# Optimization experiments

Measured on AMD Instinct MI355X. Metric: run time of the kernel, lower is better.

Reference implementation:

```python
import jax, jax.numpy as jnp
import numpy as np

DIM = 2048
N_HEADS = 32
N_KV_HEADS = 8
HEAD_DIM = DIM // N_HEADS  # 64
SEQ = 2048
BATCH = 2


def _rope_freqs(seq_len, head_dim, theta=10000.0):
    inv = 1.0 / (theta ** (np.arange(0, head_dim, 2)[: head_dim // 2].astype(np.float32) / head_dim))
    t = np.arange(seq_len, dtype=np.float32)
    ang = np.outer(t, inv)  # (seq, head_dim//2)
    return jnp.asarray(np.cos(ang)), jnp.asarray(np.sin(ang))


def setup_inputs() -> dict:
    key = jax.random.key(0)
    ks = jax.random.split(key, 5)
    x = jax.random.normal(ks[0], (BATCH, SEQ, DIM), dtype=jnp.float32)
    s = 1.0 / np.sqrt(DIM)
    wq = jax.random.normal(ks[1], (N_HEADS * HEAD_DIM, DIM), dtype=jnp.float32) * s
    wk = jax.random.normal(ks[2], (N_KV_HEADS * HEAD_DIM, DIM), dtype=jnp.float32) * s
    wv = jax.random.normal(ks[3], (N_KV_HEADS * HEAD_DIM, DIM), dtype=jnp.float32) * s
    wo = jax.random.normal(ks[4], (DIM, N_HEADS * HEAD_DIM), dtype=jnp.float32) * s
    freqs_cos, freqs_sin = _rope_freqs(SEQ, HEAD_DIM)
    return {"x": x, "freqs_cos": freqs_cos, "freqs_sin": freqs_sin,
            "wq": wq, "wk": wk, "wv": wv, "wo": wo}


def _apply_rope(t, cos, sin):
    # t: (B, S, H, D); cos/sin: (S, D//2) broadcast to (1, S, 1, D//2)
    B, S, H, D = t.shape
    tr = t.reshape(B, S, H, D // 2, 2)
    x0, x1 = tr[..., 0], tr[..., 1]
    c = cos[None, :, None, :]
    s = sin[None, :, None, :]
    o0 = x0 * c - x1 * s
    o1 = x0 * s + x1 * c
    return jnp.stack([o0, o1], axis=-1).reshape(B, S, H, D)


def reference(x, freqs_cos, freqs_sin, wq, wk, wv, wo):
    B, S, _ = x.shape
    H, KV, D = N_HEADS, N_KV_HEADS, HEAD_DIM
    rep = H // KV
    xq = jnp.einsum('bsd,hd->bsh', x, wq).reshape(B, S, H, D)
    xk = jnp.einsum('bsd,hd->bsh', x, wk).reshape(B, S, KV, D)
    xv = jnp.einsum('bsd,hd->bsh', x, wv).reshape(B, S, KV, D)
    xq = _apply_rope(xq, freqs_cos, freqs_sin)
    xk = _apply_rope(xk, freqs_cos, freqs_sin)
    # GQA without materializing repeated K/V: group q heads as (KV, rep).
    # repeat_interleave on dim=2 maps q head h -> kv head h // rep.
    xqg = xq.reshape(B, S, KV, rep, D)
    scale = 1.0 / jnp.sqrt(jnp.float32(D))
    scores = jnp.einsum('bqkrd,bskd->bkrqs', xqg, xk) * scale  # (B,KV,rep,S,S)
    causal = jnp.tril(jnp.ones((S, S), dtype=bool))
    scores = jnp.where(causal[None, None, None], scores, jnp.float32(-jnp.inf))
    probs = jax.nn.softmax(scores, axis=-1)
    out = jnp.einsum('bkrqs,bskd->bqkrd', probs, xv)  # (B,S,KV,rep,D)
    out = out.reshape(B, S, H * D)
    return jnp.einsum('bsh,dh->bsd', out, wo)
```

## Files before the change

### kernel.cpp

```cpp
#include <hip/hip_runtime.h>

#define DIMSZ 2048
#define NH 32
#define NKV 8
#define HD 64
#define SEQLEN 2048
#define BATCH 2
#define NROWS (BATCH*SEQLEN)
#define NQKVC 3072

typedef __bf16 bf16x8 __attribute__((ext_vector_type(8)));
typedef float f32x4v __attribute__((ext_vector_type(4)));

__device__ __forceinline__ unsigned short f2bf(float f) {
  union { float f; unsigned int u; } v; v.f = f;
  return (unsigned short)((v.u + 0x7FFFu + ((v.u >> 16) & 1u)) >> 16);
}
__device__ __forceinline__ float bf2f(unsigned int bits16) {
  union { unsigned int u; float f; } v; v.u = bits16 << 16; return v.f;
}
__device__ __forceinline__ int swz128(int row, int colBytes) {
  return row * 128 + (colBytes ^ ((row & 7) << 4));
}

#define GLOAD16(g, l) __builtin_amdgcn_global_load_lds( \
    (const __attribute__((address_space(1))) unsigned int*)(g), \
    (__attribute__((address_space(3))) unsigned int*)(l), 16, 0, 0)

__global__ void k_cvt(const float* __restrict__ s, unsigned short* __restrict__ d, int n4) {
  int i = blockIdx.x * 256 + threadIdx.x;
  if (i >= n4) return;
  float4 v = reinterpret_cast<const float4*>(s)[i];
  unsigned long long pk =
      (unsigned long long)f2bf(v.x) |
      ((unsigned long long)f2bf(v.y) << 16) |
      ((unsigned long long)f2bf(v.z) << 32) |
      ((unsigned long long)f2bf(v.w) << 48);
  reinterpret_cast<unsigned long long*>(d)[i] = pk;
}

__global__ void k_cvt_w(const float* __restrict__ wq, const float* __restrict__ wk,
                        const float* __restrict__ wv, unsigned short* __restrict__ d) {
  int i = blockIdx.x * 256 + threadIdx.x;
  const float* s; int off;
  if (i < 1048576)      { s = wq; off = i; }
  else if (i < 1310720) { s = wk; off = i - 1048576; }
  else                  { s = wv; off = i - 1310720; }
  float4 v = reinterpret_cast<const float4*>(s)[off];
  unsigned long long pk =
      (unsigned long long)f2bf(v.x) |
      ((unsigned long long)f2bf(v.y) << 16) |
      ((unsigned long long)f2bf(v.z) << 32) |
      ((unsigned long long)f2bf(v.w) << 48);
  reinterpret_cast<unsigned long long*>(d)[i] = pk;
}

template<int OUT_BF16>
__global__ __launch_bounds__(256, 2) void k_gemm_bt(
    const unsigned short* __restrict__ A,
    const unsigned short* __restrict__ B,
    void* __restrict__ Cv, int M, int N, int K)
{
  constexpr int BK = 64;
  __shared__ __attribute__((aligned(16))) unsigned short smA[128 * BK];
  __shared__ __attribute__((aligned(16))) unsigned short smB[128 * BK];
  const int tid = threadIdx.x;
  const int lane = tid & 63;
  const int wid = tid >> 6;
  const int lr = lane & 15, lg = lane >> 4;
  const int gx = gridDim.x;
  int lin = blockIdx.y * gx + blockIdx.x;
  const int cpx = (gx * gridDim.y) >> 3;
  lin = (lin & 7) * cpx + (lin >> 3);
  const int m0 = (lin / gx) * 128, n0 = (lin % gx) * 128;
  const int wr = (wid >> 1) * 64, wc = (wid & 1) * 64;

  f32x4v acc[4][4];
  #pragma unroll
  for (int i = 0; i < 4; i++)
    #pragma unroll
    for (int j = 0; j < 4; j++)
      acc[i][j] = f32x4v{0.f, 0.f, 0.f, 0.f};

  for (int k0 = 0; k0 < K; k0 += BK) {
    #pragma unroll
    for (int c = 0; c < 4; c++) {
      const int chunk = wid * 4 + c;
      const int idx = chunk * 64 + lane;
      const int row = idx >> 3, s = idx & 7;
      const int ks = (s ^ (row & 7)) * 8;
      GLOAD16(A + (size_t)(m0 + row) * K + k0 + ks, &smA[chunk * 512]);
      GLOAD16(B + (size_t)(n0 + row) * K + k0 + ks, &smB[chunk * 512]);
    }
    __syncthreads();
    #pragma unroll
    for (int ks = 0; ks < 2; ks++) {
      bf16x8 af[4], bfv[4];
      #pragma unroll
      for (int m = 0; m < 4; m++)
        af[m] = *reinterpret_cast<const bf16x8*>((char*)smA + swz128(wr + m * 16 + lr, ks * 64 + lg * 16));
      #pragma unroll
      for (int n = 0; n < 4; n++)
        bfv[n] = *reinterpret_cast<const bf16x8*>((char*)smB + swz128(wc + n * 16 + lr, ks * 64 + lg * 16));
      #pragma unroll
      for (int m = 0; m < 4; m++)
        #pragma unroll
        for (int n = 0; n < 4; n++)
          acc[m][n] = __builtin_amdgcn_mfma_f32_16x16x32_bf16(af[m], bfv[n], acc[m][n], 0, 0, 0);
    }
    __syncthreads();
  }
  #pragma unroll
  for (int m = 0; m < 4; m++)
    #pragma unroll
    for (int n = 0; n < 4; n++)
      #pragma unroll
      for (int r = 0; r < 4; r++) {
        const size_t row = m0 + wr + m * 16 + lg * 4 + r;
        const size_t col = n0 + wc + n * 16 + lr;
        if (OUT_BF16) ((unsigned short*)Cv)[row * N + col] = f2bf(acc[m][n][r]);
        else          ((float*)Cv)[row * N + col] = acc[m][n][r];
      }
}

__global__ void k_rope_q(const unsigned short* __restrict__ qkv,
                         const float* __restrict__ fc, const float* __restrict__ fs,
                         unsigned short* __restrict__ Qb)
{
  const int tid = blockIdx.x * 256 + threadIdx.x;
  const int i = tid & 31;
  const int t2 = tid >> 5;
  const int h = t2 & 31;
  const int row = t2 >> 5;
  const int s = row & (SEQLEN - 1);
  const int b = row >> 11;
  const unsigned int u = *reinterpret_cast<const unsigned int*>(qkv + (size_t)row * NQKVC + h * HD + 2 * i);
  const float x0 = bf2f(u & 0xffffu), x1 = bf2f(u >> 16);
  const float c = fc[s * 32 + i], sn = fs[s * 32 + i];
  const float SCL = 0.18033688011112043f;
  const float o0 = (x0 * c - x1 * sn) * SCL;
  const float o1 = (x0 * sn + x1 * c) * SCL;
  const unsigned int pk = (unsigned int)f2bf(o0) | ((unsigned int)f2bf(o1) << 16);
  *reinterpret_cast<unsigned int*>(Qb + ((size_t)((b * NH + h) * SEQLEN + s)) * HD + 2 * i) = pk;
}

__global__ void k_rope_k(const unsigned short* __restrict__ qkv,
                         const float* __restrict__ fc, const float* __restrict__ fs,
                         unsigned short* __restrict__ Kb)
{
  const int tid = blockIdx.x * 256 + threadIdx.x;
  const int i = tid & 31;
  const int t2 = tid >> 5;
  const int kv = t2 & 7;
  const int row = t2 >> 3;
  const int s = row & (SEQLEN - 1);
  const int b = row >> 11;
  const unsigned int u = *reinterpret_cast<const unsigned int*>(
      qkv + (size_t)row * NQKVC + DIMSZ + kv * HD + 2 * i);
  const float x0 = bf2f(u & 0xffffu), x1 = bf2f(u >> 16);
  const float c = fc[s * 32 + i], sn = fs[s * 32 + i];
  const float o0 = x0 * c - x1 * sn;
  const float o1 = x0 * sn + x1 * c;
  const unsigned int pk = (unsigned int)f2bf(o0) | ((unsigned int)f2bf(o1) << 16);
  *reinterpret_cast<unsigned int*>(Kb + ((size_t)((b * NKV + kv) * SEQLEN + s)) * HD + 2 * i) = pk;
}

__global__ void k_vt(const unsigned short* __restrict__ qkv, unsigned short* __restrict__ Vt) {
  __shared__ unsigned short tile[64][72];
  const int st = blockIdx.x, kv = blockIdx.y, b = blockIdx.z;
  const int tid = threadIdx.x;
  #pragma unroll
  for (int j2 = 0; j2 < 2; j2++) {
    const int s = (tid >> 3) + j2 * 32, dc = (tid & 7) * 8;
    const int row = b * SEQLEN + st * 64 + s;
    uint4 v = *reinterpret_cast<const uint4*>(
        qkv + (size_t)row * NQKVC + DIMSZ + NKV * HD + kv * HD + dc);
    const unsigned short* vs = reinterpret_cast<const unsigned short*>(&v);
    #pragma unroll
    for (int j = 0; j < 8; j++) tile[s][dc + j] = vs[j];
  }
  __syncthreads();
  {
    const int d = tid >> 2, sc = (tid & 3) * 16;
    unsigned short tmp[16];
    #pragma unroll
    for (int j = 0; j < 16; j++) tmp[j] = tile[sc + j][d];
    unsigned short* outp = Vt + ((size_t)((b * NKV + kv) * HD) + d) * SEQLEN + st * 64 + sc;
    *reinterpret_cast<uint4*>(outp)     = *reinterpret_cast<uint4*>(tmp);
    *reinterpret_cast<uint4*>(outp + 8) = *reinterpret_cast<uint4*>(tmp + 8);
  }
}

__global__ __launch_bounds__(512, 2) void k_attn(
    const unsigned short* __restrict__ Qg,
    const unsigned short* __restrict__ Kg,
    const unsigned short* __restrict__ Vt,
    unsigned short* __restrict__ Og)
{
  constexpr int KVB = 64;
  __shared__ __attribute__((aligned(16))) unsigned short sK[KVB * HD];
  __shared__ __attribute__((aligned(16))) unsigned short sV[HD * KVB];
  __shared__ __attribute__((aligned(16))) unsigned short sP[8 * 16 * KVB];
  const int tid = threadIdx.x;
  const int lane = tid & 63, wid = tid >> 6;
  const int lr = lane & 15, lg = lane >> 4;
  const int orig = blockIdx.x;
  const int w = (orig & 7) * 64 + (orig >> 3);
  const int kvh = w >> 6;
  const int b = (w >> 5) & 1;
  const int h = kvh * 4 + ((w >> 3) & 3);
  const int qp = w & 7;
  const unsigned short* Qp = Qg + ((size_t)(b * NH + h) * SEQLEN) * HD;
  const unsigned short* Kp = Kg + ((size_t)(b * NKV + kvh) * SEQLEN) * HD;
  const unsigned short* Vp = Vt + ((size_t)(b * NKV + kvh) * HD) * SEQLEN;
  unsigned short* Pw = sP + wid * (16 * KVB);

  const int sidx = wid * 64 + lane;
  const int srow = sidx >> 3;
  const int scol = ((sidx & 7) ^ (srow & 7)) * 8;

  for (int phase = 0; phase < 2; phase++) {
    const int qt = phase ? (15 - qp) : qp;
    const int qrow0 = qt * 128 + wid * 16;
    bf16x8 aq[2];
    #pragma unroll
    for (int ks = 0; ks < 2; ks++)
      aq[ks] = *reinterpret_cast<const bf16x8*>(Qp + (size_t)(qrow0 + lr) * HD + ks * 32 + lg * 8);

    f32x4v accO[4];
    #pragma unroll
    for (int r = 0; r < 4; r++) accO[r] = f32x4v{0.f, 0.f, 0.f, 0.f};
    float mrun = -3.0e38f, lrun = 0.f;

    const int nt = qt * 2 + 2;
    for (int t = 0; t < nt; t++) {
      const int kv0 = t * KVB;
      GLOAD16(Kp + (size_t)(kv0 + srow) * HD + scol, &sK[wid * 512]);
      GLOAD16(Vp + (size_t)srow * SEQLEN + kv0 + scol, &sV[wid * 512]);
      __syncthreads();
      if (kv0 <= qrow0 + 15) {
        f32x4v sfr[4];
        #pragma unroll
        for (int c = 0; c < 4; c++) sfr[c] = f32x4v{0.f, 0.f, 0.f, 0.f};
        __builtin_amdgcn_s_setprio(1);
        #pragma unroll
        for (int ks = 0; ks < 2; ks++) {
          bf16x8 bk[4];
          #pragma unroll
          for (int c = 0; c < 4; c++)
            bk[c] = *reinterpret_cast<const bf16x8*>((char*)sK + swz128(c * 16 + lr, ks * 64 + lg * 16));
          #pragma unroll
          for (int c = 0; c < 4; c++)
            sfr[c] = __builtin_amdgcn_mfma_f32_16x16x32_bf16(bk[c], aq[ks], sfr[c], 0, 0, 0);
        }
        __builtin_amdgcn_s_setprio(0);
        if (kv0 + KVB - 1 > qrow0) {
          const int q = qrow0 + lr;
          #pragma unroll
          for (int c = 0; c < 4; c++)
            #pragma unroll
            for (int r = 0; r < 4; r++) {
              const int kv = kv0 + c * 16 + lg * 4 + r;
              if (kv > q) sfr[c][r] = -1.0e30f;
            }
        }
        float mc[4];
        #pragma unroll
        for (int c = 0; c < 4; c++)
          mc[c] = fmaxf(fmaxf(sfr[c][0], sfr[c][1]), fmaxf(sfr[c][2], sfr[c][3]));
        float tm = fmaxf(fmaxf(mc[0], mc[1]), fmaxf(mc[2], mc[3]));
        tm = fmaxf(tm, __shfl_xor(tm, 16));
        tm = fmaxf(tm, __shfl_xor(tm, 32));
        const float mo = mrun;
        const bool defer = __all(tm <= mo + 8.0f);
        const float mn = defer ? mo : fmaxf(mo, tm);
        float rc[4];
        #pragma unroll
        for (int c = 0; c < 4; c++) {
          float p0 = __builtin_amdgcn_exp2f(sfr[c][0] - mn);
          float p1 = __builtin_amdgcn_exp2f(sfr[c][1] - mn);
          float p2 = __builtin_amdgcn_exp2f(sfr[c][2] - mn);
          float p3 = __builtin_amdgcn_exp2f(sfr[c][3] - mn);
          sfr[c][0] = p0; sfr[c][1] = p1; sfr[c][2] = p2; sfr[c][3] = p3;
          rc[c] = (p0 + p1) + (p2 + p3);
        }
        float rs = (rc[0] + rc[1]) + (rc[2] + rc[3]);
        rs += __shfl_xor(rs, 16);
        rs += __shfl_xor(rs, 32);
        if (defer) {
          lrun += rs;
        } else {
          const float sc = __builtin_amdgcn_exp2f(mo - mn);
          mrun = mn;
          lrun = lrun * sc + rs;
          #pragma unroll
          for (int r = 0; r < 4; r++) {
            const float scr = __shfl(sc, (lg << 4) + (lg << 2) + r);
            #pragma unroll
            for (int dc = 0; dc < 4; dc++) accO[dc][r] *= scr;
          }
        }
        #pragma unroll
        for (int c = 0; c < 4; c++) {
          uint2 pk;
          pk.x = (unsigned int)f2bf(sfr[c][0]) | ((unsigned int)f2bf(sfr[c][1]) << 16);
          pk.y = (unsigned int)f2bf(sfr[c][2]) | ((unsigned int)f2bf(sfr[c][3]) << 16);
          *reinterpret_cast<uint2*>((char*)Pw + swz128(lr, c * 32 + lg * 8)) = pk;
        }
        __builtin_amdgcn_s_setprio(1);
        #pragma unroll
        for (int ks = 0; ks < 2; ks++) {
          bf16x8 ap = *reinterpret_cast<const bf16x8*>((char*)Pw + swz128(lr, ks * 64 + lg * 16));
          bf16x8 bv[4];
          #pragma unroll
          for (int dc = 0; dc < 4; dc++)
            bv[dc] = *reinterpret_cast<const bf16x8*>((char*)sV + swz128(dc * 16 + lr, ks * 64 + lg * 16));
          #pragma unroll
          for (int dc = 0; dc < 4; dc++)
            accO[dc] = __builtin_amdgcn_mfma_f32_16x16x32_bf16(ap, bv[dc], accO[dc], 0, 0, 0);
        }
        __builtin_amdgcn_s_setprio(0);
      }
      __syncthreads();
    }
    const float inv = 1.0f / lrun;
    #pragma unroll
    for (int r = 0; r < 4; r++) {
      const float invr = __shfl(inv, (lg << 4) + (lg << 2) + r);
      const int q = qrow0 + lg * 4 + r;
      #pragma unroll
      for (int dc = 0; dc < 4; dc++) {
        const int d = dc * 16 + lr;
        Og[(size_t)(b * SEQLEN + q) * DIMSZ + h * HD + d] = f2bf(accO[dc][r] * invr);
      }
    }
  }
}

extern "C" void kernel_launch(void* const* d_in, const int* in_sizes, int n_in,
                              void* d_out, int out_size, void* d_ws, size_t ws_size,
                              hipStream_t stream)
{
  const float* x  = (const float*)d_in[0];
  const float* fc = (const float*)d_in[1];
  const float* fs = (const float*)d_in[2];
  const float* wq = (const float*)d_in[3];
  const float* wk = (const float*)d_in[4];
  const float* wv = (const float*)d_in[5];
  const float* wo = (const float*)d_in[6];
  float* out = (float*)d_out;
  char* ws = (char*)d_ws;

  unsigned short* xb    = (unsigned short*)(ws + 0);
  unsigned short* wqkvb = (unsigned short*)(ws + 16777216);
  unsigned short* wob   = (unsigned short*)(ws + 29360128);
  unsigned short* qkv   = (unsigned short*)(ws + 37748736);
  unsigned short* Qb    = (unsigned short*)(ws + 62914560);
  unsigned short* Kb    = (unsigned short*)(ws + 79691776);
  unsigned short* Vtb   = (unsigned short*)(ws + 83886080);
  unsigned short* attnb = (unsigned short*)(ws + 88080384);

  k_cvt<<<8192, 256, 0, stream>>>(x,  xb, 2097152);
  k_cvt_w<<<6144, 256, 0, stream>>>(wq, wk, wv, wqkvb);
  k_cvt<<<4096, 256, 0, stream>>>(wo, wob, 1048576);

  dim3 g1(24, 32);
  k_gemm_bt<1><<<g1, 256, 0, stream>>>(xb, wqkvb, qkv, NROWS, NQKVC, DIMSZ);

  k_rope_q<<<16384, 256, 0, stream>>>(qkv, fc, fs, Qb);
  k_rope_k<<<4096, 256, 0, stream>>>(qkv, fc, fs, Kb);
  dim3 gv(32, 8, 2);
  k_vt<<<gv, 256, 0, stream>>>(qkv, Vtb);

  k_attn<<<512, 512, 0, stream>>>(Qb, Kb, Vtb, attnb);

  dim3 g2(16, 32);
  k_gemm_bt<0><<<g2, 256, 0, stream>>>(attnb, wob, out, NROWS, DIMSZ, DIMSZ);
}
```

Measured before the change: 196.7 us.

## Double-buffer K/V tiles in attention and use hardware bf16 pack conversion

The attention kernel now keeps two LDS buffers for K and V and issues the async global-to-LDS load for the next KV tile before computing on the current one. This overlaps memory latency with MFMA and softmax work and removes one barrier per tile. It also replaces the manual round-to-nearest bf16 bit trick with compiler bf16 conversions, including a packed two-element convert, in all conversion paths. The cost is double the K/V LDS footprint, which may affect occupancy at 2 blocks per CU, and the change relies on the load-then-barrier ordering being correct.

```diff
diff --git a/kernel.cpp b/kernel.cpp
--- a/kernel.cpp
+++ b/kernel.cpp
@@ -10,11 +10,18 @@
 #define NQKVC 3072
 
 typedef __bf16 bf16x8 __attribute__((ext_vector_type(8)));
+typedef __bf16 bf16x2 __attribute__((ext_vector_type(2)));
 typedef float f32x4v __attribute__((ext_vector_type(4)));
+typedef float f32x2v __attribute__((ext_vector_type(2)));
 
 __device__ __forceinline__ unsigned short f2bf(float f) {
-  union { float f; unsigned int u; } v; v.f = f;
-  return (unsigned short)((v.u + 0x7FFFu + ((v.u >> 16) & 1u)) >> 16);
+  __bf16 h = (__bf16)f;
+  union { __bf16 h; unsigned short u; } v; v.h = h; return v.u;
+}
+__device__ __forceinline__ unsigned int pk2bf(float lo, float hi) {
+  f32x2v v; v[0] = lo; v[1] = hi;
+  bf16x2 h = __builtin_convertvector(v, bf16x2);
+  union { bf16x2 h; unsigned int u; } c; c.h = h; return c.u;
 }
 __device__ __forceinline__ float bf2f(unsigned int bits16) {
   union { unsigned int u; float f; } v; v.u = bits16 << 16; return v.f;
@@ -31,12 +38,8 @@
   int i = blockIdx.x * 256 + threadIdx.x;
   if (i >= n4) return;
   float4 v = reinterpret_cast<const float4*>(s)[i];
-  unsigned long long pk =
-      (unsigned long long)f2bf(v.x) |
-      ((unsigned long long)f2bf(v.y) << 16) |
-      ((unsigned long long)f2bf(v.z) << 32) |
-      ((unsigned long long)f2bf(v.w) << 48);
-  reinterpret_cast<unsigned long long*>(d)[i] = pk;
+  uint2 pk; pk.x = pk2bf(v.x, v.y); pk.y = pk2bf(v.z, v.w);
+  reinterpret_cast<uint2*>(d)[i] = pk;
 }
 
 __global__ void k_cvt_w(const float* __restrict__ wq, const float* __restrict__ wk,
@@ -47,12 +50,8 @@
   else if (i < 1310720) { s = wk; off = i - 1048576; }
   else                  { s = wv; off = i - 1310720; }
   float4 v = reinterpret_cast<const float4*>(s)[off];
-  unsigned long long pk =
-      (unsigned long long)f2bf(v.x) |
-      ((unsigned long long)f2bf(v.y) << 16) |
-      ((unsigned long long)f2bf(v.z) << 32) |
-      ((unsigned long long)f2bf(v.w) << 48);
-  reinterpret_cast<unsigned long long*>(d)[i] = pk;
+  uint2 pk; pk.x = pk2bf(v.x, v.y); pk.y = pk2bf(v.z, v.w);
+  reinterpret_cast<uint2*>(d)[i] = pk;
 }
 
 template<int OUT_BF16>
@@ -140,8 +139,7 @@
   const float SCL = 0.18033688011112043f;
   const float o0 = (x0 * c - x1 * sn) * SCL;
   const float o1 = (x0 * sn + x1 * c) * SCL;
-  const unsigned int pk = (unsigned int)f2bf(o0) | ((unsigned int)f2bf(o1) << 16);
-  *reinterpret_cast<unsigned int*>(Qb + ((size_t)((b * NH + h) * SEQLEN + s)) * HD + 2 * i) = pk;
+  *reinterpret_cast<unsigned int*>(Qb + ((size_t)((b * NH + h) * SEQLEN + s)) * HD + 2 * i) = pk2bf(o0, o1);
 }
 
 __global__ void k_rope_k(const unsigned short* __restrict__ qkv,
@@ -161,8 +159,7 @@
   const float c = fc[s * 32 + i], sn = fs[s * 32 + i];
   const float o0 = x0 * c - x1 * sn;
   const float o1 = x0 * sn + x1 * c;
-  const unsigned int pk = (unsigned int)f2bf(o0) | ((unsigned int)f2bf(o1) << 16);
-  *reinterpret_cast<unsigned int*>(Kb + ((size_t)((b * NKV + kv) * SEQLEN + s)) * HD + 2 * i) = pk;
+  *reinterpret_cast<unsigned int*>(Kb + ((size_t)((b * NKV + kv) * SEQLEN + s)) * HD + 2 * i) = pk2bf(o0, o1);
 }
 
 __global__ void k_vt(const unsigned short* __restrict__ qkv, unsigned short* __restrict__ Vt) {
@@ -198,8 +195,10 @@
     unsigned short* __restrict__ Og)
 {
   constexpr int KVB = 64;
-  __shared__ __attribute__((aligned(16))) unsigned short sK[KVB * HD];
-  __shared__ __attribute__((aligned(16))) unsigned short sV[HD * KVB];
+  __shared__ __attribute__((aligned(16))) unsigned short sK0[KVB * HD];
+  __shared__ __attribute__((aligned(16))) unsigned short sK1[KVB * HD];
+  __shared__ __attribute__((aligned(16))) unsigned short sV0[HD * KVB];
+  __shared__ __attribute__((aligned(16))) unsigned short sV1[HD * KVB];
   __shared__ __attribute__((aligned(16))) unsigned short sP[8 * 16 * KVB];
   const int tid = threadIdx.x;
   const int lane = tid & 63, wid = tid >> 6;
@@ -232,95 +231,109 @@
     for (int r = 0; r < 4; r++) accO[r] = f32x4v{0.f, 0.f, 0.f, 0.f};
     float mrun = -3.0e38f, lrun = 0.f;
 
-    const int nt = qt * 2 + 2;
-    for (int t = 0; t < nt; t++) {
-      const int kv0 = t * KVB;
-      GLOAD16(Kp + (size_t)(kv0 + srow) * HD + scol, &sK[wid * 512]);
-      GLOAD16(Vp + (size_t)srow * SEQLEN + kv0 + scol, &sV[wid * 512]);
-      __syncthreads();
-      if (kv0 <= qrow0 + 15) {
-        f32x4v sfr[4];
-        #pragma unroll
-        for (int c = 0; c < 4; c++) sfr[c] = f32x4v{0.f, 0.f, 0.f, 0.f};
-        __builtin_amdgcn_s_setprio(1);
-        #pragma unroll
-        for (int ks = 0; ks < 2; ks++) {
-          bf16x8 bk[4];
-          #pragma unroll
-          for (int c = 0; c < 4; c++)
-            bk[c] = *reinterpret_cast<const bf16x8*>((char*)sK + swz128(c * 16 + lr, ks * 64 + lg * 16));
-          #pragma unroll
-          for (int c = 0; c < 4; c++)
-            sfr[c] = __builtin_amdgcn_mfma_f32_16x16x32_bf16(bk[c], aq[ks], sfr[c], 0, 0, 0);
-        }
-        __builtin_amdgcn_s_setprio(0);
-        if (kv0 + KVB - 1 > qrow0) {
-          const int q = qrow0 + lr;
-          #pragma unroll
-          for (int c = 0; c < 4; c++)
-            #pragma unroll
-            for (int r = 0; r < 4; r++) {
-              const int kv = kv0 + c * 16 + lg * 4 + r;
-              if (kv > q) sfr[c][r] = -1.0e30f;
-            }
-        }
-        float mc[4];
+    auto compute = [&](int kv0, auto& sKb, auto& sVb) {
+      if (kv0 > qrow0 + 15) return;
+      f32x4v sfr[4];
+      #pragma unroll
+      for (int c = 0; c < 4; c++) sfr[c] = f32x4v{0.f, 0.f, 0.f, 0.f};
+      __builtin_amdgcn_s_setprio(1);
+      #pragma unroll
+      for (int ks = 0; ks < 2; ks++) {
+        bf16x8 bk[4];
         #pragma unroll
         for (int c = 0; c < 4; c++)
-          mc[c] = fmaxf(fmaxf(sfr[c][0], sfr[c][1]), fmaxf(sfr[c][2], sfr[c][3]));
-        float tm = fmaxf(fmaxf(mc[0], mc[1]), fmaxf(mc[2], mc[3]));
-        tm = fmaxf(tm, __shfl_xor(tm, 16));
-        tm = fmaxf(tm, __shfl_xor(tm, 32));
-        const float mo = mrun;
-        const bool defer = __all(tm <= mo + 8.0f);
-        const float mn = defer ? mo : fmaxf(mo, tm);
-        float rc[4];
-        #pragma unroll
-        for (int c = 0; c < 4; c++) {
-          float p0 = __builtin_amdgcn_exp2f(sfr[c][0] - mn);
-          float p1 = __builtin_amdgcn_exp2f(sfr[c][1] - mn);
-          float p2 = __builtin_amdgcn_exp2f(sfr[c][2] - mn);
-          float p3 = __builtin_amdgcn_exp2f(sfr[c][3] - mn);
-          sfr[c][0] = p0; sfr[c][1] = p1; sfr[c][2] = p2; sfr[c][3] = p3;
-          rc[c] = (p0 + p1) + (p2 + p3);
-        }
-        float rs = (rc[0] + rc[1]) + (rc[2] + rc[3]);
-        rs += __shfl_xor(rs, 16);
-        rs += __shfl_xor(rs, 32);
-        if (defer) {
-          lrun += rs;
-        } else {
-          const float sc = __builtin_amdgcn_exp2f(mo - mn);
-          mrun = mn;
-          lrun = lrun * sc + rs;
+          bk[c] = *reinterpret_cast<const bf16x8*>((char*)sKb + swz128(c * 16 + lr, ks * 64 + lg * 16));
+        #pragma unroll
+        for (int c = 0; c < 4; c++)
+          sfr[c] = __builtin_amdgcn_mfma_f32_16x16x32_bf16(bk[c], aq[ks], sfr[c], 0, 0, 0);
+      }
+      __builtin_amdgcn_s_setprio(0);
+      if (kv0 + KVB - 1 > qrow0) {
+        const int q = qrow0 + lr;
+        #pragma unroll
+        for (int c = 0; c < 4; c++)
           #pragma unroll
           for (int r = 0; r < 4; r++) {
-            const float scr = __shfl(sc, (lg << 4) + (lg << 2) + r);
-            #pragma unroll
-            for (int dc = 0; dc < 4; dc++) accO[dc][r] *= scr;
+            const int kv = kv0 + c * 16 + lg * 4 + r;
+            if (kv > q) sfr[c][r] = -1.0e30f;
           }
+      }
+      float mc[4];
+      #pragma unroll
+      for (int c = 0; c < 4; c++)
+        mc[c] = fmaxf(fmaxf(sfr[c][0], sfr[c][1]), fmaxf(sfr[c][2], sfr[c][3]));
+      float tm = fmaxf(fmaxf(mc[0], mc[1]), fmaxf(mc[2], mc[3]));
+      tm = fmaxf(tm, __shfl_xor(tm, 16));
+      tm = fmaxf(tm, __shfl_xor(tm, 32));
+      const float mo = mrun;
+      const bool defer = __all(tm <= mo + 8.0f);
+      const float mn = defer ? mo : fmaxf(mo, tm);
+      float rc[4];
+      #pragma unroll
+      for (int c = 0; c < 4; c++) {
+        float p0 = __builtin_amdgcn_exp2f(sfr[c][0] - mn);
+        float p1 = __builtin_amdgcn_exp2f(sfr[c][1] - mn);
+        float p2 = __builtin_amdgcn_exp2f(sfr[c][2] - mn);
+        float p3 = __builtin_amdgcn_exp2f(sfr[c][3] - mn);
+        sfr[c][0] = p0; sfr[c][1] = p1; sfr[c][2] = p2; sfr[c][3] = p3;
+        rc[c] = (p0 + p1) + (p2 + p3);
+      }
+      float rs = (rc[0] + rc[1]) + (rc[2] + rc[3]);
+      rs += __shfl_xor(rs, 16);
+      rs += __shfl_xor(rs, 32);
+      if (defer) {
+        lrun += rs;
+      } else {
+        const float sc = __builtin_amdgcn_exp2f(mo - mn);
+        mrun = mn;
+        lrun = lrun * sc + rs;
+        #pragma unroll
+        for (int r = 0; r < 4; r++) {
+          const float scr = __shfl(sc, (lg << 4) + (lg << 2) + r);
+          #pragma unroll
+          for (int dc = 0; dc < 4; dc++) accO[dc][r] *= scr;
         }
-        #pragma unroll
-        for (int c = 0; c < 4; c++) {
-          uint2 pk;
-          pk.x = (unsigned int)f2bf(sfr[c][0]) | ((unsigned int)f2bf(sfr[c][1]) << 16);
-          pk.y = (unsigned int)f2bf(sfr[c][2]) | ((unsigned int)f2bf(sfr[c][3]) << 16);
-          *reinterpret_cast<uint2*>((char*)Pw + swz128(lr, c * 32 + lg * 8)) = pk;
-        }
-        __builtin_amdgcn_s_setprio(1);
-        #pragma unroll
-        for (int ks = 0; ks < 2; ks++) {
-          bf16x8 ap = *reinterpret_cast<const bf16x8*>((char*)Pw + swz128(lr, ks * 64 + lg * 16));
-          bf16x8 bv[4];
-          #pragma unroll
-          for (int dc = 0; dc < 4; dc++)
-            bv[dc] = *reinterpret_cast<const bf16x8*>((char*)sV + swz128(dc * 16 + lr, ks * 64 + lg * 16));
-          #pragma unroll
-          for (int dc = 0; dc < 4; dc++)
-            accO[dc] = __builtin_amdgcn_mfma_f32_16x16x32_bf16(ap, bv[dc], accO[dc], 0, 0, 0);
-        }
-        __builtin_amdgcn_s_setprio(0);
-      }
+      }
+      #pragma unroll
+      for (int c = 0; c < 4; c++) {
+        uint2 pk;
+        pk.x = pk2bf(sfr[c][0], sfr[c][1]);
+        pk.y = pk2bf(sfr[c][2], sfr[c][3]);
+        *reinterpret_cast<uint2*>((char*)Pw + swz128(lr, c * 32 + lg * 8)) = pk;
+      }
+      __builtin_amdgcn_s_setprio(1);
+      #pragma unroll
+      for (int ks = 0; ks < 2; ks++) {
+        bf16x8 ap = *reinterpret_cast<const bf16x8*>((char*)Pw + swz128(lr, ks * 64 + lg * 16));
+        bf16x8 bv[4];
+        #pragma unroll
+        for (int dc = 0; dc < 4; dc++)
+          bv[dc] = *reinterpret_cast<const bf16x8*>((char*)sVb + swz128(dc * 16 + lr, ks * 64 + lg * 16));
+        #pragma unroll
+        for (int dc = 0; dc < 4; dc++)
+          accO[dc] = __builtin_amdgcn_mfma_f32_16x16x32_bf16(ap, bv[dc], accO[dc], 0, 0, 0);
+      }
+      __builtin_amdgcn_s_setprio(0);
+    };
+
+    const int nt = qt * 2 + 2;
+    GLOAD16(Kp + (size_t)srow * HD + scol, &sK0[wid * 512]);
+    GLOAD16(Vp + (size_t)srow * SEQLEN + scol, &sV0[wid * 512]);
+    __syncthreads();
+    for (int t = 0; t < nt; t += 2) {
+      {
+        const int kn = (t + 1) * KVB;
+        GLOAD16(Kp + (size_t)(kn + srow) * HD + scol, &sK1[wid * 512]);
+        GLOAD16(Vp + (size_t)srow * SEQLEN + kn + scol, &sV1[wid * 512]);
+      }
+      compute(t * KVB, sK0, sV0);
+      __syncthreads();
+      if (t + 2 < nt) {
+        const int kn = (t + 2) * KVB;
+        GLOAD16(Kp + (size_t)(kn + srow) * HD + scol, &sK0[wid * 512]);
+        GLOAD16(Vp + (size_t)srow * SEQLEN + kn + scol, &sV0[wid * 512]);
+      }
+      compute((t + 1) * KVB, sK1, sV1);
       __syncthreads();
     }
     const float inv = 1.0f / lrun;
```

Result: faster. 186.5 us (-5.2%).
